# Kernel optimization log

Measured on AMD Instinct MI355X. Metric: run time of the kernel, lower is better.

## Reference

```python
import jax, jax.numpy as jnp
import numpy as np

OUT_C, IN_C, K = 64, 64, 3
H, W = 32, 32


def setup_inputs() -> dict:
    key = jax.random.key(0)
    k1, k2, k3 = jax.random.split(key, 3)
    x = jax.random.normal(k1, (1, H, W, IN_C), dtype=jnp.float32)
    # One rational activation (P5/Q4, PAU 'version A') per (out_c, in_c, ky, kx)
    w_num = jax.random.normal(k2, (OUT_C, IN_C, K, K, 6), dtype=jnp.float32) * 0.1
    w_den = jax.random.normal(k3, (OUT_C, IN_C, K, K, 4), dtype=jnp.float32) * 0.1
    return {"x": x, "w_num": w_num, "w_den": w_den}


def reference(x, w_num, w_den):
    # x: [1, H, W, C] -- original module only supports batch=1 (squeeze semantics)
    h, w, c = x.shape[1], x.shape[2], x.shape[3]
    pad = (K - 1) // 2
    xp = jnp.pad(x[0], ((pad, pad), (pad, pad), (0, 0)))  # [H+2p, W+2p, C]
    # patches[a,b,i,j,c] = xp[i+a, j+b, c]  (same 'same-padding' sliding window)
    patches = jnp.stack(
        [jnp.stack([xp[a:a + h, b:b + w, :] for b in range(K)], axis=0)
         for a in range(K)], axis=0)  # [K,K,H,W,C]
    # powers x^0..x^5, computed once and reused by numerator and denominator
    pows = jnp.stack([patches ** n for n in range(6)], axis=0)  # [6,K,K,H,W,C]
    # per (f,c,a,b) rational: P(x) = sum_n a_n x^n,  Q(x) = 1 + |sum_{n=1..4} b_n x^n|
    P = jnp.einsum('nabijc,fcabn->fabijc', pows, w_num)
    Q = 1.0 + jnp.abs(jnp.einsum('nabijc,fcabn->fabijc', pows[1:5], w_den))
    # sum contributions over kernel positions (a,b) and input channels c
    return jnp.sum(P / Q, axis=(1, 2, 5))  # [OUT_C, H, W]
```

## Files before the change

### kernel.cpp

```cpp
#include <hip/hip_runtime.h>
#include <math.h>

#define NOUT 64
#define NIN  64
#define HH   32
#define WW   32
#define XSTR 137

__global__ __launch_bounds__(512, 8) void kan_main(const float* __restrict__ x,
                                                   const float* __restrict__ wn,
                                                   const float* __restrict__ wd,
                                                   float* __restrict__ out) {
    __shared__ float xt[NIN * XSTR];
    __shared__ float red[512];

    int bid  = blockIdx.x;
    int wgid = (bid & 7) * 128 + (bid >> 3);
    int f    = wgid >> 4;
    int band = wgid & 15;
    int i0   = band * 2;

    int tid = threadIdx.x;

#pragma unroll
    for (int k = 0; k < 17; ++k) {
        int idx = k * 512 + tid;
        int c   = idx & 63;
        int pos = idx >> 6;
        int t   = pos / 34;
        int col = pos % 34;
        int gi  = i0 - 1 + t;
        int gj  = col - 1;
        float v = 0.0f;
        if (gi >= 0 && gi < HH && gj >= 0 && gj < WW)
            v = x[(gi * WW + gj) * NIN + c];
        xt[c * XSTR + pos] = v;
    }
    __syncthreads();

    int lane = tid & 63;
    int wv   = __builtin_amdgcn_readfirstlane(tid >> 6);
    int r    = lane >> 5;
    int j    = lane & 31;

    float acc = 0.0f;

    const float* wnf = wn + (size_t)(f * NIN + wv * 8) * 54;
    const float* wdf = wd + (size_t)(f * NIN + wv * 8) * 36;

    for (int cc = 0; cc < 8; ++cc) {
        const float* wnc = wnf + cc * 54;
        const float* wdc = wdf + cc * 36;
        const float* xc  = &xt[(wv * 8 + cc) * XSTR + r * 34 + j];
#pragma unroll
        for (int a = 0; a < 3; ++a) {
#pragma unroll
            for (int b = 0; b < 3; ++b) {
                const int ab = a * 3 + b;
                float xv = xc[a * 34 + b];
                float pn = fmaf(wnc[ab * 6 + 5], xv, wnc[ab * 6 + 4]);
                pn = fmaf(pn, xv, wnc[ab * 6 + 3]);
                pn = fmaf(pn, xv, wnc[ab * 6 + 2]);
                pn = fmaf(pn, xv, wnc[ab * 6 + 1]);
                pn = fmaf(pn, xv, wnc[ab * 6 + 0]);
                float qn = fmaf(wdc[ab * 4 + 3], xv, wdc[ab * 4 + 2]);
                qn = fmaf(qn, xv, wdc[ab * 4 + 1]);
                qn = fmaf(qn, xv, wdc[ab * 4 + 0]);
                float den = 1.0f + fabsf(xv * qn);
                acc = fmaf(pn, __builtin_amdgcn_rcpf(den), acc);
            }
        }
    }

    red[tid] = acc;
    __syncthreads();
    if (tid < 64) {
        float s = red[tid]       + red[tid + 64]  + red[tid + 128] + red[tid + 192]
                + red[tid + 256] + red[tid + 320] + red[tid + 384] + red[tid + 448];
        int rr = tid >> 5;
        int jj = tid & 31;
        out[f * (HH * WW) + (i0 + rr) * WW + jj] = s;
    }
}

extern "C" void kernel_launch(void* const* d_in, const int* in_sizes, int n_in,
                              void* d_out, int out_size, void* d_ws, size_t ws_size,
                              hipStream_t stream) {
    const float* x  = (const float*)d_in[0];
    const float* wn = (const float*)d_in[1];
    const float* wd = (const float*)d_in[2];
    float* out = (float*)d_out;
    (void)d_ws; (void)ws_size;

    kan_main<<<1024, 512, 0, stream>>>(x, wn, wd, out);
}
```

Measured before the change: 23.59 us.

## Compute two output rows per thread with 4-row bands to reuse weights

Each block now covers a 4-row band instead of 2, halving the block count, and each thread computes two output rows. Each weight load then serves two positions. Weights are loaded as float2/float4 vectors, and the reduction reuses the input tile's shared memory. The cost is more shared memory per block (larger halo tile), lower occupancy (launch bounds 6), fewer blocks in flight, and loss of the readfirstlane hint, so the weight loads may no longer be scalar.

```diff
diff --git a/kernel.cpp b/kernel.cpp
--- a/kernel.cpp
+++ b/kernel.cpp
@@ -5,81 +5,112 @@
 #define NIN  64
 #define HH   32
 #define WW   32
-#define XSTR 137
+#define CSTR 204
+#define NBLK 512
 
-__global__ __launch_bounds__(512, 8) void kan_main(const float* __restrict__ x,
+__global__ __launch_bounds__(512, 6) void kan_main(const float* __restrict__ x,
                                                    const float* __restrict__ wn,
                                                    const float* __restrict__ wd,
                                                    float* __restrict__ out) {
-    __shared__ float xt[NIN * XSTR];
-    __shared__ float red[512];
+    __shared__ float xt[NIN * CSTR];
 
     int bid  = blockIdx.x;
-    int wgid = (bid & 7) * 128 + (bid >> 3);
-    int f    = wgid >> 4;
-    int band = wgid & 15;
-    int i0   = band * 2;
+    int wgid = (bid & 7) * (NBLK / 8) + (bid >> 3);
+    int f    = wgid >> 3;
+    int band = wgid & 7;
+    int i0   = band * 4;
 
     int tid = threadIdx.x;
 
-#pragma unroll
-    for (int k = 0; k < 17; ++k) {
+    for (int k = 0; k < 26; ++k) {
         int idx = k * 512 + tid;
-        int c   = idx & 63;
-        int pos = idx >> 6;
-        int t   = pos / 34;
-        int col = pos % 34;
-        int gi  = i0 - 1 + t;
-        int gj  = col - 1;
-        float v = 0.0f;
-        if (gi >= 0 && gi < HH && gj >= 0 && gj < WW)
-            v = x[(gi * WW + gj) * NIN + c];
-        xt[c * XSTR + pos] = v;
+        if (idx < NIN * CSTR) {
+            int c   = idx & 63;
+            int pos = idx >> 6;
+            int row = pos / 34;
+            int col = pos % 34;
+            int gi  = i0 - 1 + row;
+            int gj  = col - 1;
+            float v = 0.0f;
+            if (gi >= 0 && gi < HH && gj >= 0 && gj < WW)
+                v = x[(gi * WW + gj) * NIN + c];
+            xt[c * CSTR + pos] = v;
+        }
     }
     __syncthreads();
 
     int lane = tid & 63;
-    int wv   = __builtin_amdgcn_readfirstlane(tid >> 6);
-    int r    = lane >> 5;
+    int wv   = tid >> 6;
+    int r2   = lane >> 5;
     int j    = lane & 31;
 
-    float acc = 0.0f;
-
-    const float* wnf = wn + (size_t)(f * NIN + wv * 8) * 54;
-    const float* wdf = wd + (size_t)(f * NIN + wv * 8) * 36;
+    float acc0 = 0.0f, acc1 = 0.0f;
+    int cbase = wv * 8;
 
     for (int cc = 0; cc < 8; ++cc) {
-        const float* wnc = wnf + cc * 54;
-        const float* wdc = wdf + cc * 36;
-        const float* xc  = &xt[(wv * 8 + cc) * XSTR + r * 34 + j];
+        int c = cbase + cc;
+
+        const float* xb = &xt[c * CSTR + (r2 * 2) * 34 + j];
+        float xw[4][3];
+#pragma unroll
+        for (int dr = 0; dr < 4; ++dr)
+#pragma unroll
+            for (int dc = 0; dc < 3; ++dc)
+                xw[dr][dc] = xb[dr * 34 + dc];
+
+        size_t rec = (size_t)(f * NIN + c);
+        const float2* wn2 = (const float2*)(wn + rec * 54);
+        const float4* wd4 = (const float4*)(wd + rec * 36);
+
 #pragma unroll
         for (int a = 0; a < 3; ++a) {
 #pragma unroll
             for (int b = 0; b < 3; ++b) {
                 const int ab = a * 3 + b;
-                float xv = xc[a * 34 + b];
-                float pn = fmaf(wnc[ab * 6 + 5], xv, wnc[ab * 6 + 4]);
-                pn = fmaf(pn, xv, wnc[ab * 6 + 3]);
-                pn = fmaf(pn, xv, wnc[ab * 6 + 2]);
-                pn = fmaf(pn, xv, wnc[ab * 6 + 1]);
-                pn = fmaf(pn, xv, wnc[ab * 6 + 0]);
-                float qn = fmaf(wdc[ab * 4 + 3], xv, wdc[ab * 4 + 2]);
-                qn = fmaf(qn, xv, wdc[ab * 4 + 1]);
-                qn = fmaf(qn, xv, wdc[ab * 4 + 0]);
-                float den = 1.0f + fabsf(xv * qn);
-                acc = fmaf(pn, __builtin_amdgcn_rcpf(den), acc);
+                float2 A01 = wn2[ab * 3 + 0];
+                float2 A23 = wn2[ab * 3 + 1];
+                float2 A45 = wn2[ab * 3 + 2];
+                float4 Bq  = wd4[ab];
+                {
+                    float xv = xw[a][b];
+                    float p = fmaf(A45.y, xv, A45.x);
+                    p = fmaf(p, xv, A23.y);
+                    p = fmaf(p, xv, A23.x);
+                    p = fmaf(p, xv, A01.y);
+                    p = fmaf(p, xv, A01.x);
+                    float q = fmaf(Bq.w, xv, Bq.z);
+                    q = fmaf(q, xv, Bq.y);
+                    q = fmaf(q, xv, Bq.x);
+                    float den = 1.0f + fabsf(xv * q);
+                    acc0 = fmaf(p, __builtin_amdgcn_rcpf(den), acc0);
+                }
+                {
+                    float xv = xw[a + 1][b];
+                    float p = fmaf(A45.y, xv, A45.x);
+                    p = fmaf(p, xv, A23.y);
+                    p = fmaf(p, xv, A23.x);
+                    p = fmaf(p, xv, A01.y);
+                    p = fmaf(p, xv, A01.x);
+                    float q = fmaf(Bq.w, xv, Bq.z);
+                    q = fmaf(q, xv, Bq.y);
+                    q = fmaf(q, xv, Bq.x);
+                    float den = 1.0f + fabsf(xv * q);
+                    acc1 = fmaf(p, __builtin_amdgcn_rcpf(den), acc1);
+                }
             }
         }
     }
 
-    red[tid] = acc;
     __syncthreads();
-    if (tid < 64) {
-        float s = red[tid]       + red[tid + 64]  + red[tid + 128] + red[tid + 192]
-                + red[tid + 256] + red[tid + 320] + red[tid + 384] + red[tid + 448];
-        int rr = tid >> 5;
-        int jj = tid & 31;
-        out[f * (HH * WW) + (i0 + rr) * WW + jj] = s;
+    float* red = xt;
+    red[wv * 128 + (r2 * 2 + 0) * 32 + j] = acc0;
+    red[wv * 128 + (r2 * 2 + 1) * 32 + j] = acc1;
+    __syncthreads();
+    if (tid < 128) {
+        float s = 0.0f;
+#pragma unroll
+        for (int w = 0; w < 8; ++w) s += red[w * 128 + tid];
+        out[f * (HH * WW) + (i0 + (tid >> 5)) * WW + (tid & 31)] = s;
     }
 }
 
@@ -90,7 +121,7 @@
     const float* wn = (const float*)d_in[1];
     const float* wd = (const float*)d_in[2];
     float* out = (float*)d_out;
-    (void)d_ws; (void)ws_size;
+    (void)d_ws; (void)ws_size; (void)in_sizes; (void)n_in; (void)out_size;
 
-    kan_main<<<1024, 512, 0, stream>>>(x, wn, wd, out);
+    kan_main<<<NBLK, 512, 0, stream>>>(x, wn, wd, out);
 }
```

Result: slower. 32.15 us (+36.3%).

## Stage rational weights in LDS and process four rows per 1024-thread block

Applied to the files above, without the earlier changes.

Blocks grow to 1024 threads covering four output rows per filter, which halves the grid and lowers redundant halo loads of the input tile. All of one filter's numerator and denominator coefficients are copied into shared memory, padded to 12-float records so they can be read as float4 vectors, rather than fetched as scalar global loads per channel. The reduction buffer reuses the weight LDS region. The extra shared memory (about 105 KB) and larger blocks limit occupancy, and the weight staging adds setup work per block.

```diff
diff --git a/kernel.cpp b/kernel.cpp
--- a/kernel.cpp
+++ b/kernel.cpp
@@ -5,81 +5,116 @@
 #define NIN  64
 #define HH   32
 #define WW   32
-#define XSTR 137
+#define XCPL 205
+#define XROWS 6
+#define XCOLS 34
+#define XWORDS (XROWS * XCOLS * NIN)
+#define WREC 12
+#define NBLK 512
 
-__global__ __launch_bounds__(512, 8) void kan_main(const float* __restrict__ x,
-                                                   const float* __restrict__ wn,
-                                                   const float* __restrict__ wd,
-                                                   float* __restrict__ out) {
-    __shared__ float xt[NIN * XSTR];
-    __shared__ float red[512];
+typedef float f4 __attribute__((ext_vector_type(4)));
+
+__global__ __launch_bounds__(1024, 8) void kan_main(const float* __restrict__ x,
+                                                    const float* __restrict__ wn,
+                                                    const float* __restrict__ wd,
+                                                    float* __restrict__ out) {
+    __shared__ float xt[NIN * XCPL];
+    __shared__ __align__(16) float wl[NIN * 9 * WREC];
 
     int bid  = blockIdx.x;
-    int wgid = (bid & 7) * 128 + (bid >> 3);
-    int f    = wgid >> 4;
-    int band = wgid & 15;
-    int i0   = band * 2;
+    int wgid = (bid & 7) * (NBLK / 8) + (bid >> 3);
+    int f    = wgid >> 3;
+    int band = wgid & 7;
+    int i0   = band * 4;
 
     int tid = threadIdx.x;
 
-#pragma unroll
-    for (int k = 0; k < 17; ++k) {
-        int idx = k * 512 + tid;
-        int c   = idx & 63;
-        int pos = idx >> 6;
-        int t   = pos / 34;
-        int col = pos % 34;
-        int gi  = i0 - 1 + t;
-        int gj  = col - 1;
-        float v = 0.0f;
-        if (gi >= 0 && gi < HH && gj >= 0 && gj < WW)
-            v = x[(gi * WW + gj) * NIN + c];
-        xt[c * XSTR + pos] = v;
+    for (int k = 0; k < 13; ++k) {
+        int idx = k * 1024 + tid;
+        if (idx < XWORDS) {
+            int c   = idx & 63;
+            int t   = idx >> 6;
+            int row = t / 34;
+            int col = t % 34;
+            int gi  = i0 - 1 + row;
+            int gj  = col - 1;
+            float v = 0.0f;
+            if (gi >= 0 && gi < HH && gj >= 0 && gj < WW)
+                v = x[(gi * WW + gj) * NIN + c];
+            xt[c * XCPL + row * 34 + col] = v;
+        }
+    }
+    const float* wnf = wn + (size_t)f * (NIN * 54);
+    for (int k = 0; k < 4; ++k) {
+        int t = k * 1024 + tid;
+        if (t < NIN * 54) {
+            int c   = t / 54;
+            int rem = t - c * 54;
+            int ab  = rem / 6;
+            int n   = rem - ab * 6;
+            wl[(c * 9 + ab) * WREC + n] = wnf[t];
+        }
+    }
+    const float* wdf = wd + (size_t)f * (NIN * 36);
+    for (int k = 0; k < 3; ++k) {
+        int t = k * 1024 + tid;
+        if (t < NIN * 36) {
+            int c   = t / 36;
+            int rem = t - c * 36;
+            int ab  = rem / 4;
+            int n   = rem - ab * 4;
+            wl[(c * 9 + ab) * WREC + 6 + n] = wdf[t];
+        }
     }
     __syncthreads();
 
     int lane = tid & 63;
     int wv   = __builtin_amdgcn_readfirstlane(tid >> 6);
-    int r    = lane >> 5;
+    int cgrp = wv & 7;
+    int half = wv >> 3;
+    int r    = half * 2 + (lane >> 5);
     int j    = lane & 31;
 
     float acc = 0.0f;
 
-    const float* wnf = wn + (size_t)(f * NIN + wv * 8) * 54;
-    const float* wdf = wd + (size_t)(f * NIN + wv * 8) * 36;
+#pragma unroll
+    for (int cc = 0; cc < 8; ++cc) {
+        int c = cgrp * 8 + cc;
+        const float* xb = &xt[c * XCPL + r * 34 + j];
+        float xw[9];
+        xw[0] = xb[0];  xw[1] = xb[1];  xw[2] = xb[2];
+        xw[3] = xb[34]; xw[4] = xb[35]; xw[5] = xb[36];
+        xw[6] = xb[68]; xw[7] = xb[69]; xw[8] = xb[70];
 
-    for (int cc = 0; cc < 8; ++cc) {
-        const float* wnc = wnf + cc * 54;
-        const float* wdc = wdf + cc * 36;
-        const float* xc  = &xt[(wv * 8 + cc) * XSTR + r * 34 + j];
+        const f4* wr = (const f4*)&wl[c * 9 * WREC];
 #pragma unroll
-        for (int a = 0; a < 3; ++a) {
-#pragma unroll
-            for (int b = 0; b < 3; ++b) {
-                const int ab = a * 3 + b;
-                float xv = xc[a * 34 + b];
-                float pn = fmaf(wnc[ab * 6 + 5], xv, wnc[ab * 6 + 4]);
-                pn = fmaf(pn, xv, wnc[ab * 6 + 3]);
-                pn = fmaf(pn, xv, wnc[ab * 6 + 2]);
-                pn = fmaf(pn, xv, wnc[ab * 6 + 1]);
-                pn = fmaf(pn, xv, wnc[ab * 6 + 0]);
-                float qn = fmaf(wdc[ab * 4 + 3], xv, wdc[ab * 4 + 2]);
-                qn = fmaf(qn, xv, wdc[ab * 4 + 1]);
-                qn = fmaf(qn, xv, wdc[ab * 4 + 0]);
-                float den = 1.0f + fabsf(xv * qn);
-                acc = fmaf(pn, __builtin_amdgcn_rcpf(den), acc);
-            }
+        for (int ab = 0; ab < 9; ++ab) {
+            f4 w0 = wr[ab * 3 + 0];
+            f4 w1 = wr[ab * 3 + 1];
+            f4 w2 = wr[ab * 3 + 2];
+            float xv = xw[ab];
+            float p = fmaf(w1.y, xv, w1.x);
+            p = fmaf(p, xv, w0.w);
+            p = fmaf(p, xv, w0.z);
+            p = fmaf(p, xv, w0.y);
+            p = fmaf(p, xv, w0.x);
+            float q = fmaf(w2.y, xv, w2.x);
+            q = fmaf(q, xv, w1.w);
+            q = fmaf(q, xv, w1.z);
+            float den = 1.0f + fabsf(xv * q);
+            acc = fmaf(p, __builtin_amdgcn_rcpf(den), acc);
         }
     }
 
-    red[tid] = acc;
     __syncthreads();
-    if (tid < 64) {
-        float s = red[tid]       + red[tid + 64]  + red[tid + 128] + red[tid + 192]
-                + red[tid + 256] + red[tid + 320] + red[tid + 384] + red[tid + 448];
-        int rr = tid >> 5;
-        int jj = tid & 31;
-        out[f * (HH * WW) + (i0 + rr) * WW + jj] = s;
+    float* red = wl;
+    red[cgrp * 128 + r * 32 + j] = acc;
+    __syncthreads();
+    if (tid < 128) {
+        float s = 0.0f;
+#pragma unroll
+        for (int g = 0; g < 8; ++g) s += red[g * 128 + tid];
+        out[f * (HH * WW) + i0 * WW + tid] = s;
     }
 }
 
@@ -90,7 +125,7 @@
     const float* wn = (const float*)d_in[1];
     const float* wd = (const float*)d_in[2];
     float* out = (float*)d_out;
-    (void)d_ws; (void)ws_size;
+    (void)d_ws; (void)ws_size; (void)in_sizes; (void)n_in; (void)out_size;
 
-    kan_main<<<1024, 512, 0, stream>>>(x, wn, wd, out);
+    kan_main<<<NBLK, 1024, 0, stream>>>(x, wn, wd, out);
 }
```

New measurement: 24.11 us. 1.02x slower.
